# Optimization experiments

Hardware: AMD Instinct MI355X
Metric: run time of the kernel (lower is better)

## Reference

```python
import jax, jax.numpy as jnp
import numpy as np

L_CHUNK = 5   # frames per camera chunk (hardcoded L=5 in similarity())
N_CAMS = 6    # len(cam_list)
TOP_K = 8     # hardcoded K=8 in similarity()
HEADS = 8


def setup_inputs() -> dict:
    key = jax.random.key(0)
    ks = jax.random.split(key, 5)
    B, M, N, C = 1, L_CHUNK * N_CAMS, 261, 2048  # M = S*P = 30 multiview token groups
    scale = 0.02
    tokens = jax.random.normal(ks[0], (B, M, N, C), dtype=jnp.float32)
    Wq = jax.random.normal(ks[1], (C, C), dtype=jnp.float32) * scale
    Wk = jax.random.normal(ks[2], (C, C), dtype=jnp.float32) * scale
    Wv = jax.random.normal(ks[3], (C, C), dtype=jnp.float32) * scale
    Wo = jax.random.normal(ks[4], (C, C), dtype=jnp.float32) * scale
    return {"tokens": tokens, "Wq": Wq, "Wk": Wk, "Wv": Wv, "Wo": Wo}


def _similarity(pose_tokens):
    # pose_tokens: [B, M, C] -> block-diag-biased softmax sim + topk neighbors
    sim = jnp.einsum('bmc,bnc->bmn', pose_tokens, pose_tokens)
    block = jnp.kron(jnp.eye(N_CAMS, dtype=sim.dtype),
                     jnp.ones((L_CHUNK, L_CHUNK), dtype=sim.dtype))  # [M, M]
    sim = sim + 10000.0 * block
    probs = jax.nn.softmax(sim, axis=-1)
    vals, idx = jax.lax.top_k(probs, TOP_K)  # [B, M, K]
    return vals, idx


def reference(tokens, Wq, Wk, Wv, Wo):
    B, M, N, C = tokens.shape
    H = HEADS
    d = C // H
    # similarity + topk over camera/pose tokens (token index 0 of each group)
    vals, idx = _similarity(tokens[:, :, 0, :])
    # gather K neighbor token groups per (batch, group): [B, M, K, N, C]
    nbr = jax.vmap(lambda t, i: t[i])(tokens, idx)
    nbr = nbr.reshape(B, M, TOP_K * N, C)
    q = (tokens @ Wq).reshape(B, M, N, H, d)
    k = (nbr @ Wk).reshape(B, M, TOP_K * N, H, d)
    v = (nbr @ Wv).reshape(B, M, TOP_K * N, H, d)
    scores = jnp.einsum('bmqhd,bmkhd->bmhqk', q, k) / jnp.sqrt(jnp.asarray(d, q.dtype))
    # weight each neighbor's tokens by its topk similarity value (log-bias)
    bias = jnp.repeat(jnp.log(vals + 1e-6), N, axis=-1)  # [B, M, K*N]
    scores = scores + bias[:, :, None, None, :]
    attn = jax.nn.softmax(scores, axis=-1)
    out = jnp.einsum('bmhqk,bmkhd->bmqhd', attn, v).reshape(B, M, N, C)
    return tokens + out @ Wo
```

## Files before the change

### kernel.cpp

```cpp
#include <hip/hip_runtime.h>
#include <stdint.h>

#define MTOK 7830
#define MPAD 7936
#define CD   2048
#define VTC  7920
#define AS1 __attribute__((address_space(1)))
#define AS3 __attribute__((address_space(3)))

typedef unsigned short u16;
typedef __bf16 bf16x8 __attribute__((ext_vector_type(8)));
typedef float f32x4 __attribute__((ext_vector_type(4)));
typedef unsigned short u16x8 __attribute__((ext_vector_type(8)));

__device__ __forceinline__ u16 f2bf(float f) {
  unsigned x = __float_as_uint(f);
  return (u16)((x + 0x7fffu + ((x >> 16) & 1u)) >> 16);
}

__device__ __forceinline__ void gld16(const u16* g, u16* l) {
  __builtin_amdgcn_global_load_lds((AS1 const unsigned int*)(g), (AS3 unsigned int*)(l), 16, 0, 0);
}

__global__ void cvt_tokens(const float* __restrict__ T, u16* __restrict__ O) {
  int row = blockIdx.x;
  size_t base = (size_t)row * CD + threadIdx.x * 8;
  u16x8 o = {0,0,0,0,0,0,0,0};
  if (row < MTOK) {
    const float* s = T + base;
    #pragma unroll
    for (int j = 0; j < 8; ++j) o[j] = f2bf(s[j]);
  }
  *(u16x8*)&O[base] = o;
}

__global__ void cvt_w(const float* __restrict__ Wq, const float* __restrict__ Wk,
                      const float* __restrict__ Wv, const float* __restrict__ Wo,
                      u16* __restrict__ WqkvT, u16* __restrict__ WoT) {
  __shared__ float tile[32][33];
  int k0 = blockIdx.x * 32;
  int n0 = blockIdx.y * 32;
  const float* W; u16* Dst; int nl0, dr0;
  if (n0 < 2048)      { W = Wq; Dst = WqkvT; nl0 = n0;        dr0 = n0; }
  else if (n0 < 4096) { W = Wk; Dst = WqkvT; nl0 = n0 - 2048; dr0 = n0; }
  else if (n0 < 6144) { W = Wv; Dst = WqkvT; nl0 = n0 - 4096; dr0 = n0; }
  else                { W = Wo; Dst = WoT;   nl0 = n0 - 6144; dr0 = n0 - 6144; }
  int tx = threadIdx.x, ty = threadIdx.y;
  #pragma unroll
  for (int i = 0; i < 4; ++i)
    tile[ty + i*8][tx] = W[(size_t)(k0 + ty + i*8) * CD + nl0 + tx];
  __syncthreads();
  #pragma unroll
  for (int i = 0; i < 4; ++i) {
    int n = ty + i*8;
    Dst[(size_t)(dr0 + n) * CD + k0 + tx] = f2bf(tile[tx][n]);
  }
}

__global__ void posesim(const float* __restrict__ tok, float* __restrict__ sim) {
  int mm = blockIdx.y, nn = blockIdx.x;
  const float* a = tok + (size_t)mm * 261 * CD;
  const float* b = tok + (size_t)nn * 261 * CD;
  int tid = threadIdx.x;
  float p = 0.f;
  for (int j = tid; j < CD; j += 256) p += a[j] * b[j];
  __shared__ float red[256];
  red[tid] = p; __syncthreads();
  for (int s = 128; s > 0; s >>= 1) { if (tid < s) red[tid] += red[tid + s]; __syncthreads(); }
  if (tid == 0) sim[mm*30 + nn] = red[0] + (((mm/5) == (nn/5)) ? 10000.0f : 0.0f);
}

__global__ void topk_bias(const float* __restrict__ sim, float* __restrict__ bias,
                          int* __restrict__ idxo) {
  int m = threadIdx.x;
  if (m >= 30) return;
  float p[30];
  float mx = -1e30f;
  for (int j = 0; j < 30; ++j) { p[j] = sim[m*30 + j]; mx = fmaxf(mx, p[j]); }
  float z = 0.f;
  for (int j = 0; j < 30; ++j) { p[j] = __expf(p[j] - mx); z += p[j]; }
  float inv = 1.0f / z;
  for (int j = 0; j < 30; ++j) p[j] *= inv;
  for (int k = 0; k < 8; ++k) {
    int bj = 0; float bv = p[0];
    for (int j = 1; j < 30; ++j) if (p[j] > bv) { bv = p[j]; bj = j; }
    idxo[m*8 + k] = bj;
    bias[m*8 + k] = logf(bv + 1e-6f);
    p[bj] = -1.0f;
  }
}

template<int EPI>
__global__ __launch_bounds__(512) void gemm_bt(
    const u16* __restrict__ A, const u16* __restrict__ Bt,
    u16* __restrict__ Cq, u16* __restrict__ Cv,
    const float* __restrict__ resid, float* __restrict__ Dout, int K)
{
  __shared__ u16 Al[2][256 * 64];
  __shared__ u16 Bl[2][256 * 64];
  int tid = threadIdx.x, lane = tid & 63, wid = tid >> 6;
  int lo4 = lane & 15, hi2 = lane >> 4;
  int lin = blockIdx.y * gridDim.x + blockIdx.x;
  int q8  = (gridDim.x * gridDim.y) >> 3;
  int lin2 = (lin & 7) * q8 + (lin >> 3);
  int bn = lin2 % gridDim.x, bm = lin2 / gridDim.x;
  int wy = wid >> 2, wx = wid & 3;
  int r8 = lane >> 3, c8 = lane & 7;

  f32x4 acc[8][4] = {};

  size_t aofs[4], bofs[4];
  #pragma unroll
  for (int j = 0; j < 4; ++j) {
    int row = wid*32 + j*8 + r8;
    int sw = 8 * (c8 ^ (row & 7));
    aofs[j] = (size_t)(bm*256 + row) * K + sw;
    bofs[j] = (size_t)(bn*256 + row) * K + sw;
  }
  int ldst = wid * 2048;

  int nK = K >> 6;
  #pragma unroll
  for (int j = 0; j < 4; ++j) {
    gld16(A  + aofs[j], &Al[0][ldst + j*512]);
    gld16(Bt + bofs[j], &Bl[0][ldst + j*512]);
  }
  #pragma unroll
  for (int j = 0; j < 4; ++j) {
    gld16(A  + 64 + aofs[j], &Al[1][ldst + j*512]);
    gld16(Bt + 64 + bofs[j], &Bl[1][ldst + j*512]);
  }

  for (int t = 0; t < nK; ++t) {
    if (t + 1 < nK) asm volatile("s_waitcnt vmcnt(8)" ::: "memory");
    else            asm volatile("s_waitcnt vmcnt(0)" ::: "memory");
    __builtin_amdgcn_sched_barrier(0);
    __builtin_amdgcn_s_barrier();
    __builtin_amdgcn_sched_barrier(0);

    const u16* Ac = Al[t & 1];
    const u16* Bc = Bl[t & 1];

    bf16x8 bv[4][2];
    #pragma unroll
    for (int ni = 0; ni < 4; ++ni) {
      int br = wx*64 + ni*16 + lo4;
      #pragma unroll
      for (int kk = 0; kk < 2; ++kk)
        bv[ni][kk] = *(const bf16x8*)&Bc[br*64 + 8*((kk*4 + hi2) ^ (br & 7))];
    }

    #pragma unroll
    for (int mg = 0; mg < 2; ++mg) {
      bf16x8 av[4][2];
      #pragma unroll
      for (int mi = 0; mi < 4; ++mi) {
        int ar = wy*128 + mg*64 + mi*16 + lo4;
        #pragma unroll
        for (int kk = 0; kk < 2; ++kk)
          av[mi][kk] = *(const bf16x8*)&Ac[ar*64 + 8*((kk*4 + hi2) ^ (ar & 7))];
      }
      __builtin_amdgcn_s_setprio(1);
      #pragma unroll
      for (int kk = 0; kk < 2; ++kk)
        #pragma unroll
        for (int mi = 0; mi < 4; ++mi)
          #pragma unroll
          for (int ni = 0; ni < 4; ++ni)
            acc[mg*4 + mi][ni] = __builtin_amdgcn_mfma_f32_16x16x32_bf16(
                av[mi][kk], bv[ni][kk], acc[mg*4 + mi][ni], 0, 0, 0);
      __builtin_amdgcn_s_setprio(0);
      if (mg == 0) {
        __builtin_amdgcn_s_barrier();
      } else {
        __builtin_amdgcn_sched_barrier(0);
        if (t + 2 < nK) {
          size_t kn = (size_t)(t + 2) << 6;
          u16* An = Al[t & 1];
          u16* Bn = Bl[t & 1];
          #pragma unroll
          for (int j = 0; j < 4; ++j) {
            gld16(A  + kn + aofs[j], &An[ldst + j*512]);
            gld16(Bt + kn + bofs[j], &Bn[ldst + j*512]);
          }
        }
        __builtin_amdgcn_sched_barrier(0);
      }
    }
  }

  int gm0 = bm*256 + wy*128;
  int gn0 = bn*256 + wx*64;
  #pragma unroll
  for (int mi = 0; mi < 8; ++mi) {
    #pragma unroll
    for (int ni = 0; ni < 4; ++ni) {
      int gmb = gm0 + mi*16 + hi2*4;
      int gn  = gn0 + ni*16 + lo4;
      #pragma unroll
      for (int r = 0; r < 4; ++r) {
        float v = acc[mi][ni][r];
        int gm = gmb + r;
        if (EPI == 0) {
          if (gn < 4096) {
            Cq[(size_t)gm * 4096 + gn] = f2bf(v);
          } else if (gm < MTOK) {
            int g = gm / 261, tk = gm - g * 261;
            Cv[(size_t)(gn - 4096) * VTC + g * 264 + tk] = f2bf(v);
          }
        } else {
          if (gm < MTOK) {
            size_t off = (size_t)gm * CD + gn;
            Dout[off] = resid[off] + v;
          }
        }
      }
    }
  }
}

__global__ __launch_bounds__(512) void attn_main(
    const u16* __restrict__ QK,
    const u16* __restrict__ VtG,
    const float* __restrict__ bias, const int* __restrict__ idx,
    u16* __restrict__ AO)
{
  int h = blockIdx.x, m = blockIdx.y;
  int tid = threadIdx.x, lane = tid & 63, wid = tid >> 6;
  int lo4 = lane & 15, hi2 = lane >> 4;

  __shared__ u16 Kl[2][32 * 256];
  __shared__ u16 Vl[2][256 * 32];
  __shared__ u16 Pl[8][2][16 * 50];
  __shared__ float bias_s[8];
  __shared__ int   idx_s[8];
  if (tid < 8) {
    bias_s[tid] = bias[m*8 + tid] * 1.4426950408889634f;
    idx_s[tid]  = idx[m*8 + tid];
  }

  bf16x8 qf[2][8];
  #pragma unroll
  for (int qg = 0; qg < 2; ++qg) {
    int qrow = m*261 + wid*32 + qg*16 + lo4;
    #pragma unroll
    for (int kk = 0; kk < 8; ++kk)
      qf[qg][kk] = *(const bf16x8*)&QK[(size_t)qrow * 4096 + h*256 + kk*32 + hi2*8];
  }

  size_t kofs[2], vofs[2];
  #pragma unroll
  for (int i = 0; i < 2; ++i) {
    int rt = 4*wid + 2*i + (lane >> 5);
    kofs[i] = (size_t)rt * 4096 + 2048 + h*256 + 8*((lane & 31) ^ (rt & 7));
    int vdr = 32*wid + 16*i + (lane >> 2);
    vofs[i] = (size_t)(h*256 + vdr) * VTC + 8*((lane & 3) ^ ((vdr >> 1) & 3));
  }
  int ld0 = wid * 1024;

  f32x4 O[2][16] = {};
  float srun[2][4] = {};
  const float SC = 0.09016844f;

  {
    int ig0 = idx[m*8];
    #pragma unroll
    for (int i = 0; i < 2; ++i) {
      gld16(QK + (size_t)(ig0*261) * 4096 + kofs[i], &Kl[0][ld0 + i*512]);
      gld16(VtG + (size_t)(ig0*264) + vofs[i],       &Vl[0][ld0 + i*512]);
    }
  }

  int vswz = 8 * (hi2 ^ ((lo4 >> 1) & 3));
  int kxb  = (lo4 >> 2) & 1;
  int kswz = 8 * (hi2 ^ (lo4 & 3));

  for (int it = 0; it < 72; ++it) {
    __syncthreads();
    if (it + 1 < 72) {
      int tn = it + 1;
      int gg = tn / 9;
      int tok0n = (tn - gg*9) * 32;
      int ign = idx_s[gg];
      #pragma unroll
      for (int i = 0; i < 2; ++i) {
        gld16(QK + (size_t)(ign*261 + tok0n) * 4096 + kofs[i], &Kl[tn & 1][ld0 + i*512]);
        gld16(VtG + (size_t)(ign*264 + tok0n) + vofs[i],       &Vl[tn & 1][ld0 + i*512]);
      }
    }
    {
      int gg = it / 9;
      int tok0 = (it - gg*9) * 32;
      float bgl = bias_s[gg];
      const u16* Kb = Kl[it & 1];
      const u16* Vb = Vl[it & 1];

      f32x4 sv[2][2] = {};
      __builtin_amdgcn_s_setprio(1);
      #pragma unroll
      for (int kk = 0; kk < 8; ++kk) {
        int off = lo4*256 + 32*(kk ^ kxb) + kswz;
        bf16x8 kb0 = *(const bf16x8*)&Kb[off];
        bf16x8 kb1 = *(const bf16x8*)&Kb[off + 16*256];
        sv[0][0] = __builtin_amdgcn_mfma_f32_16x16x32_bf16(qf[0][kk], kb0, sv[0][0], 0, 0, 0);
        sv[0][1] = __builtin_amdgcn_mfma_f32_16x16x32_bf16(qf[0][kk], kb1, sv[0][1], 0, 0, 0);
        sv[1][0] = __builtin_amdgcn_mfma_f32_16x16x32_bf16(qf[1][kk], kb0, sv[1][0], 0, 0, 0);
        sv[1][1] = __builtin_amdgcn_mfma_f32_16x16x32_bf16(qf[1][kk], kb1, sv[1][1], 0, 0, 0);
      }
      __builtin_amdgcn_s_setprio(0);
      bool v0 = (tok0 + lo4) < 261, v1 = (tok0 + 16 + lo4) < 261;
      #pragma unroll
      for (int qg = 0; qg < 2; ++qg) {
        u16* Pw = Pl[wid][qg];
        #pragma unroll
        for (int r = 0; r < 4; ++r) {
          float e0 = __builtin_exp2f(fmaf(sv[qg][0][r], SC, bgl));
          float e1 = __builtin_exp2f(fmaf(sv[qg][1][r], SC, bgl));
          e0 = v0 ? e0 : 0.f;
          e1 = v1 ? e1 : 0.f;
          srun[qg][r] += e0 + e1;
          Pw[(hi2*4 + r)*50 + lo4]      = f2bf(e0);
          Pw[(hi2*4 + r)*50 + 16 + lo4] = f2bf(e1);
        }
      }
      bf16x8 pa0 = *(const bf16x8*)&Pl[wid][0][lo4*50 + hi2*8];
      bf16x8 pa1 = *(const bf16x8*)&Pl[wid][1][lo4*50 + hi2*8];
      __builtin_amdgcn_s_setprio(1);
      #pragma unroll
      for (int o = 0; o < 16; ++o) {
        bf16x8 vv = *(const bf16x8*)&Vb[(o*16 + lo4)*32 + vswz];
        O[0][o] = __builtin_amdgcn_mfma_f32_16x16x32_bf16(pa0, vv, O[0][o], 0, 0, 0);
        O[1][o] = __builtin_amdgcn_mfma_f32_16x16x32_bf16(pa1, vv, O[1][o], 0, 0, 0);
      }
      __builtin_amdgcn_s_setprio(0);
    }
  }

  #pragma unroll
  for (int qg = 0; qg < 2; ++qg) {
    float inv[4];
    #pragma unroll
    for (int r = 0; r < 4; ++r) {
      float s = srun[qg][r];
      s += __shfl_xor(s, 1);
      s += __shfl_xor(s, 2);
      s += __shfl_xor(s, 4);
      s += __shfl_xor(s, 8);
      inv[r] = 1.0f / s;
    }
    #pragma unroll
    for (int o = 0; o < 16; ++o) {
      #pragma unroll
      for (int r = 0; r < 4; ++r) {
        int qq = wid*32 + qg*16 + hi2*4 + r;
        AO[(size_t)(m*261 + qq) * CD + h*256 + o*16 + lo4] = f2bf(O[qg][o][r] * inv[r]);
      }
    }
  }
}

__global__ __launch_bounds__(256) void attn_tail(
    const u16* __restrict__ QK, const u16* __restrict__ VtG,
    const float* __restrict__ bias, const int* __restrict__ idx,
    u16* __restrict__ AO)
{
  int h = blockIdx.x, m = blockIdx.y;
  int tid = threadIdx.x, lane = tid & 63, wid = tid >> 6;
  int lo4 = lane & 15, hi2 = lane >> 4;

  __shared__ float Om[4][16][256];
  __shared__ float Sm[4][16];
  __shared__ u16 Pl[4][16 * 50];

  int q = 256 + lo4;
  bool qv = q < 261;
  int qrow = m*261 + (qv ? q : 0);
  bf16x8 qf[8];
  #pragma unroll
  for (int kk = 0; kk < 8; ++kk) {
    u16x8 u = {0,0,0,0,0,0,0,0};
    if (qv) u = *(const u16x8*)&QK[(size_t)qrow * 4096 + h*256 + kk*32 + hi2*8];
    qf[kk] = __builtin_bit_cast(bf16x8, u);
  }

  f32x4 O[16] = {};
  float srun[4] = {0.f, 0.f, 0.f, 0.f};
  const float SC = 0.09016844f;

  for (int it = wid; it < 72; it += 4) {
    int gg = it / 9;
    int tok0 = (it - gg*9) * 32;
    int ig = idx[m*8 + gg];
    float bgl = bias[m*8 + gg] * 1.4426950408889634f;
    const u16* kbase = QK + (size_t)(ig*261 + tok0) * 4096 + 2048 + h*256;
    f32x4 s0v = {0,0,0,0}, s1v = {0,0,0,0};
    #pragma unroll
    for (int kk = 0; kk < 8; ++kk) {
      bf16x8 kb0 = *(const bf16x8*)&kbase[(size_t)lo4 * 4096 + kk*32 + hi2*8];
      bf16x8 kb1 = *(const bf16x8*)&kbase[(size_t)(16 + lo4) * 4096 + kk*32 + hi2*8];
      s0v = __builtin_amdgcn_mfma_f32_16x16x32_bf16(qf[kk], kb0, s0v, 0, 0, 0);
      s1v = __builtin_amdgcn_mfma_f32_16x16x32_bf16(qf[kk], kb1, s1v, 0, 0, 0);
    }
    bool v0 = (tok0 + lo4) < 261, v1 = (tok0 + 16 + lo4) < 261;
    float p0[4], p1[4];
    #pragma unroll
    for (int r = 0; r < 4; ++r) {
      float e0 = __builtin_exp2f(fmaf(s0v[r], SC, bgl));
      float e1 = __builtin_exp2f(fmaf(s1v[r], SC, bgl));
      e0 = v0 ? e0 : 0.f;
      e1 = v1 ? e1 : 0.f;
      srun[r] += e0 + e1;
      p0[r] = e0; p1[r] = e1;
    }
    u16* Pw = Pl[wid];
    #pragma unroll
    for (int r = 0; r < 4; ++r) {
      Pw[(hi2*4 + r)*50 + lo4]      = f2bf(p0[r]);
      Pw[(hi2*4 + r)*50 + 16 + lo4] = f2bf(p1[r]);
    }
    bf16x8 pa = *(const bf16x8*)&Pw[lo4*50 + hi2*8];
    const u16* vbase = VtG + (size_t)(h*256) * VTC + ig*264 + tok0;
    #pragma unroll
    for (int o = 0; o < 16; ++o) {
      bf16x8 vv = *(const bf16x8*)&vbase[(size_t)(o*16 + lo4) * VTC + hi2*8];
      O[o] = __builtin_amdgcn_mfma_f32_16x16x32_bf16(pa, vv, O[o], 0, 0, 0);
    }
  }

  #pragma unroll
  for (int r = 0; r < 4; ++r) {
    float s = srun[r];
    s += __shfl_xor(s, 1);
    s += __shfl_xor(s, 2);
    s += __shfl_xor(s, 4);
    s += __shfl_xor(s, 8);
    srun[r] = s;
  }
  #pragma unroll
  for (int o = 0; o < 16; ++o)
    #pragma unroll
    for (int r = 0; r < 4; ++r)
      Om[wid][hi2*4 + r][o*16 + lo4] = O[o][r];
  if (lo4 == 0) {
    #pragma unroll
    for (int r = 0; r < 4; ++r) Sm[wid][hi2*4 + r] = srun[r];
  }
  __syncthreads();
  if (wid == 0) {
    #pragma unroll
    for (int o = 0; o < 16; ++o) {
      #pragma unroll
      for (int r = 0; r < 4; ++r) {
        int row = hi2*4 + r;
        int qq = 256 + row;
        if (qq < 261) {
          int c = o*16 + lo4;
          float v = Om[0][row][c] + Om[1][row][c] + Om[2][row][c] + Om[3][row][c];
          float s = Sm[0][row] + Sm[1][row] + Sm[2][row] + Sm[3][row];
          AO[(size_t)(m*261 + qq) * CD + h*256 + c] = f2bf(v / s);
        }
      }
    }
  }
}

extern "C" void kernel_launch(void* const* d_in, const int* in_sizes, int n_in,
                              void* d_out, int out_size, void* d_ws, size_t ws_size,
                              hipStream_t stream) {
  const float* tokens = (const float*)d_in[0];
  const float* Wq = (const float*)d_in[1];
  const float* Wk = (const float*)d_in[2];
  const float* Wv = (const float*)d_in[3];
  const float* Wo = (const float*)d_in[4];
  float* out = (float*)d_out;
  char* ws = (char*)d_ws;

  constexpr size_t OFF_TOKBF = 0;
  constexpr size_t OFF_WQKVT = OFF_TOKBF + (size_t)MPAD * CD * 2;
  constexpr size_t OFF_WOT   = OFF_WQKVT + (size_t)6144 * CD * 2;
  constexpr size_t OFF_QK    = OFF_WOT   + (size_t)CD * CD * 2;
  constexpr size_t OFF_VTG   = OFF_QK    + (size_t)MPAD * 4096 * 2;
  constexpr size_t OFF_AO    = OFF_VTG   + (size_t)CD * VTC * 2 + 4096;
  constexpr size_t OFF_SIM   = OFF_AO    + (size_t)MPAD * CD * 2;
  constexpr size_t OFF_BIAS  = OFF_SIM   + 4096;
  constexpr size_t OFF_IDX   = OFF_BIAS  + 1024;

  u16* tokBf  = (u16*)(ws + OFF_TOKBF);
  u16* WqkvT  = (u16*)(ws + OFF_WQKVT);
  u16* WoT    = (u16*)(ws + OFF_WOT);
  u16* QKbuf  = (u16*)(ws + OFF_QK);
  u16* VtG    = (u16*)(ws + OFF_VTG);
  u16* attnO  = (u16*)(ws + OFF_AO);
  float* simw = (float*)(ws + OFF_SIM);
  float* bw   = (float*)(ws + OFF_BIAS);
  int*   iw   = (int*)(ws + OFF_IDX);

  cvt_tokens<<<MPAD, 256, 0, stream>>>(tokens, tokBf);
  cvt_w<<<dim3(64, 256), dim3(32, 8), 0, stream>>>(Wq, Wk, Wv, Wo, WqkvT, WoT);
  posesim<<<dim3(30, 30), 256, 0, stream>>>(tokens, simw);
  topk_bias<<<1, 32, 0, stream>>>(simw, bw, iw);
  gemm_bt<0><<<dim3(24, 31), 512, 0, stream>>>(tokBf, WqkvT, QKbuf, VtG, nullptr, nullptr, CD);
  attn_tail<<<dim3(8, 30), 256, 0, stream>>>(QKbuf, VtG, bw, iw, attnO);
  attn_main<<<dim3(8, 30), 512, 0, stream>>>(QKbuf, VtG, bw, iw, attnO);
  gemm_bt<1><<<dim3(8, 31), 512, 0, stream>>>(attnO, WoT, nullptr, nullptr, tokens, out, CD);
}
```

Measured before the change: 640.4 us.

## Use 4 waves with 128x128 per-wave tiles in GEMM

The GEMM block drops from 8 waves to 4 waves, and each wave now computes a 128x128 output tile (8x8 MFMA fragments) instead of 128x64. This raises register reuse of the A/B fragments loaded from LDS and removes the mid-iteration barrier, leaving one barrier per k-step before issuing the next prefetch. The cost is that each thread now holds 256 accumulator floats. This risks register spilling or an AGPR-heavy allocation, and it halves the number of waves available to hide latency.

```diff
diff --git a/kernel.cpp b/kernel.cpp
--- a/kernel.cpp
+++ b/kernel.cpp
@@ -91,7 +91,7 @@
 }
 
 template<int EPI>
-__global__ __launch_bounds__(512) void gemm_bt(
+__global__ __launch_bounds__(256, 1) void gemm_bt(
     const u16* __restrict__ A, const u16* __restrict__ Bt,
     u16* __restrict__ Cq, u16* __restrict__ Cv,
     const float* __restrict__ resid, float* __restrict__ Dout, int K)
@@ -104,35 +104,35 @@
   int q8  = (gridDim.x * gridDim.y) >> 3;
   int lin2 = (lin & 7) * q8 + (lin >> 3);
   int bn = lin2 % gridDim.x, bm = lin2 / gridDim.x;
-  int wy = wid >> 2, wx = wid & 3;
+  int wy = wid >> 1, wx = wid & 1;
   int r8 = lane >> 3, c8 = lane & 7;
 
-  f32x4 acc[8][4] = {};
-
-  size_t aofs[4], bofs[4];
-  #pragma unroll
-  for (int j = 0; j < 4; ++j) {
-    int row = wid*32 + j*8 + r8;
+  f32x4 acc[8][8] = {};
+
+  size_t aofs[8], bofs[8];
+  #pragma unroll
+  for (int j = 0; j < 8; ++j) {
+    int row = wid*64 + j*8 + r8;
     int sw = 8 * (c8 ^ (row & 7));
     aofs[j] = (size_t)(bm*256 + row) * K + sw;
     bofs[j] = (size_t)(bn*256 + row) * K + sw;
   }
-  int ldst = wid * 2048;
+  int ldst = wid * 4096;
 
   int nK = K >> 6;
   #pragma unroll
-  for (int j = 0; j < 4; ++j) {
+  for (int j = 0; j < 8; ++j) {
     gld16(A  + aofs[j], &Al[0][ldst + j*512]);
     gld16(Bt + bofs[j], &Bl[0][ldst + j*512]);
   }
   #pragma unroll
-  for (int j = 0; j < 4; ++j) {
+  for (int j = 0; j < 8; ++j) {
     gld16(A  + 64 + aofs[j], &Al[1][ldst + j*512]);
     gld16(Bt + 64 + bofs[j], &Bl[1][ldst + j*512]);
   }
 
   for (int t = 0; t < nK; ++t) {
-    if (t + 1 < nK) asm volatile("s_waitcnt vmcnt(8)" ::: "memory");
+    if (t + 1 < nK) asm volatile("s_waitcnt vmcnt(16)" ::: "memory");
     else            asm volatile("s_waitcnt vmcnt(0)" ::: "memory");
     __builtin_amdgcn_sched_barrier(0);
     __builtin_amdgcn_s_barrier();
@@ -141,60 +141,48 @@
     const u16* Ac = Al[t & 1];
     const u16* Bc = Bl[t & 1];
 
-    bf16x8 bv[4][2];
-    #pragma unroll
-    for (int ni = 0; ni < 4; ++ni) {
-      int br = wx*64 + ni*16 + lo4;
-      #pragma unroll
-      for (int kk = 0; kk < 2; ++kk)
-        bv[ni][kk] = *(const bf16x8*)&Bc[br*64 + 8*((kk*4 + hi2) ^ (br & 7))];
-    }
-
-    #pragma unroll
-    for (int mg = 0; mg < 2; ++mg) {
-      bf16x8 av[4][2];
-      #pragma unroll
-      for (int mi = 0; mi < 4; ++mi) {
-        int ar = wy*128 + mg*64 + mi*16 + lo4;
+    #pragma unroll
+    for (int kk = 0; kk < 2; ++kk) {
+      bf16x8 av[8], bv[8];
+      #pragma unroll
+      for (int i = 0; i < 8; ++i) {
+        int ar = wy*128 + i*16 + lo4;
+        av[i] = *(const bf16x8*)&Ac[ar*64 + 8*((kk*4 + hi2) ^ (ar & 7))];
+        int br = wx*128 + i*16 + lo4;
+        bv[i] = *(const bf16x8*)&Bc[br*64 + 8*((kk*4 + hi2) ^ (br & 7))];
+      }
+      __builtin_amdgcn_s_setprio(1);
+      #pragma unroll
+      for (int mi = 0; mi < 8; ++mi)
         #pragma unroll
-        for (int kk = 0; kk < 2; ++kk)
-          av[mi][kk] = *(const bf16x8*)&Ac[ar*64 + 8*((kk*4 + hi2) ^ (ar & 7))];
-      }
-      __builtin_amdgcn_s_setprio(1);
-      #pragma unroll
-      for (int kk = 0; kk < 2; ++kk)
-        #pragma unroll
-        for (int mi = 0; mi < 4; ++mi)
-          #pragma unroll
-          for (int ni = 0; ni < 4; ++ni)
-            acc[mg*4 + mi][ni] = __builtin_amdgcn_mfma_f32_16x16x32_bf16(
-                av[mi][kk], bv[ni][kk], acc[mg*4 + mi][ni], 0, 0, 0);
+        for (int ni = 0; ni < 8; ++ni)
+          acc[mi][ni] = __builtin_amdgcn_mfma_f32_16x16x32_bf16(
+              av[mi], bv[ni], acc[mi][ni], 0, 0, 0);
       __builtin_amdgcn_s_setprio(0);
-      if (mg == 0) {
-        __builtin_amdgcn_s_barrier();
-      } else {
-        __builtin_amdgcn_sched_barrier(0);
-        if (t + 2 < nK) {
-          size_t kn = (size_t)(t + 2) << 6;
-          u16* An = Al[t & 1];
-          u16* Bn = Bl[t & 1];
-          #pragma unroll
-          for (int j = 0; j < 4; ++j) {
-            gld16(A  + kn + aofs[j], &An[ldst + j*512]);
-            gld16(Bt + kn + bofs[j], &Bn[ldst + j*512]);
-          }
-        }
-        __builtin_amdgcn_sched_barrier(0);
-      }
+    }
+
+    __builtin_amdgcn_sched_barrier(0);
+    __builtin_amdgcn_s_barrier();
+    __builtin_amdgcn_sched_barrier(0);
+    if (t + 2 < nK) {
+      size_t kn = (size_t)(t + 2) << 6;
+      u16* An = Al[t & 1];
+      u16* Bn = Bl[t & 1];
+      #pragma unroll
+      for (int j = 0; j < 8; ++j) {
+        gld16(A  + kn + aofs[j], &An[ldst + j*512]);
+        gld16(Bt + kn + bofs[j], &Bn[ldst + j*512]);
+      }
+      __builtin_amdgcn_sched_barrier(0);
     }
   }
 
   int gm0 = bm*256 + wy*128;
-  int gn0 = bn*256 + wx*64;
+  int gn0 = bn*256 + wx*128;
   #pragma unroll
   for (int mi = 0; mi < 8; ++mi) {
     #pragma unroll
-    for (int ni = 0; ni < 4; ++ni) {
+    for (int ni = 0; ni < 8; ++ni) {
       int gmb = gm0 + mi*16 + hi2*4;
       int gn  = gn0 + ni*16 + lo4;
       #pragma unroll
@@ -499,8 +487,8 @@
   cvt_w<<<dim3(64, 256), dim3(32, 8), 0, stream>>>(Wq, Wk, Wv, Wo, WqkvT, WoT);
   posesim<<<dim3(30, 30), 256, 0, stream>>>(tokens, simw);
   topk_bias<<<1, 32, 0, stream>>>(simw, bw, iw);
-  gemm_bt<0><<<dim3(24, 31), 512, 0, stream>>>(tokBf, WqkvT, QKbuf, VtG, nullptr, nullptr, CD);
+  gemm_bt<0><<<dim3(24, 31), 256, 0, stream>>>(tokBf, WqkvT, QKbuf, VtG, nullptr, nullptr, CD);
   attn_tail<<<dim3(8, 30), 256, 0, stream>>>(QKbuf, VtG, bw, iw, attnO);
   attn_main<<<dim3(8, 30), 512, 0, stream>>>(QKbuf, VtG, bw, iw, attnO);
-  gemm_bt<1><<<dim3(8, 31), 512, 0, stream>>>(attnO, WoT, nullptr, nullptr, tokens, out, CD);
-}
+  gemm_bt<1><<<dim3(8, 31), 256, 0, stream>>>(attnO, WoT, nullptr, nullptr, tokens, out, CD);
+}
```

After: 757.4 us. 1.18x slower.
